# Kernel optimization log

Measured on AMD Instinct MI355X. Metric: run time of the kernel, lower is better.

Reference implementation:

```python
import jax, jax.numpy as jnp
import numpy as np

B, N, C_CLASS, C_CHARGE, S_MAX = 128, 256, 5, 3, 300


def setup_inputs() -> dict:
    key = jax.random.key(0)
    ks = jax.random.split(key, 12)
    return {
        "particle_class": jax.random.randint(ks[0], (B, N), 0, C_CLASS),
        "particle_charge": jax.random.randint(ks[1], (B, N), 0, C_CHARGE),
        "n_particles": jax.random.randint(ks[2], (B,), 0, S_MAX),
        "pflow_class_logits": jax.random.normal(ks[3], (B, N, C_CLASS), jnp.float32),
        "pflow_charge_logits": jax.random.normal(ks[4], (B, N, C_CHARGE), jnp.float32),
        "particle_pos": jax.random.normal(ks[5], (B, N, 3), jnp.float32),
        "pflow_pos": jax.random.normal(ks[6], (B, N, 3), jnp.float32),
        "particle_mom": jax.random.normal(ks[7], (B, N, 3), jnp.float32),
        "pflow_mom": jax.random.normal(ks[8], (B, N, 3), jnp.float32),
        "particle_energy": jax.random.normal(ks[9], (B, N), jnp.float32),
        "pflow_energy": jax.random.normal(ks[10], (B, N), jnp.float32),
        "predicted_setsizes": jax.random.normal(ks[11], (B, N, S_MAX), jnp.float32),
    }


def _pairwise_nll(logits, labels):
    # logits: [B, Nq, C] (pflow/dst side), labels: [B, Np] int (particle/src side)
    # returns CE(dst_logits_j, src_label_i) for every pair -> [B, Np, Nq]
    logp = jax.nn.log_softmax(logits, axis=-1)            # [B, Nq, C]
    idx = labels[:, :, None, None]                        # [B, Np, 1, 1]
    return -jnp.take_along_axis(logp[:, None, :, :], idx, axis=3)[..., 0]


def reference(particle_class, particle_charge, n_particles,
              pflow_class_logits, pflow_charge_logits,
              particle_pos, pflow_pos, particle_mom, pflow_mom,
              particle_energy, pflow_energy, predicted_setsizes):
    # per-edge (full bipartite per event) pair losses -> [B, Np, Nq]
    class_l = _pairwise_nll(pflow_class_logits, particle_class)
    charge_l = _pairwise_nll(pflow_charge_logits, particle_charge)
    pos_l = jnp.linalg.norm(particle_pos[:, :, None, :] - pflow_pos[:, None, :, :], axis=-1)
    mom_l = jnp.linalg.norm(particle_mom[:, :, None, :] - pflow_mom[:, None, :, :], axis=-1)
    en_l = (particle_energy[:, :, None] - pflow_energy[:, None, :]) ** 2
    pair_loss = class_l + charge_l + pos_l + mom_l + en_l  # [B, Np, Nq]

    # segment-min over mailbox: per-pflow min over incoming particle edges,
    # per-particle min over incoming pflow edges
    min_per_pflow = pair_loss.min(axis=1)      # [B, Nq]
    min_per_particle = pair_loss.min(axis=2)   # [B, Np]

    particle_loss = min_per_particle.sum(axis=1).mean()
    pflow_loss = min_per_pflow.sum(axis=1).mean()

    # setsize: mean over pflow nodes per event, CE against true multiplicity
    setsize_logp = jax.nn.log_softmax(predicted_setsizes.mean(axis=1), axis=-1)  # [B, S]
    setsize_loss = -jnp.take_along_axis(setsize_logp, n_particles[:, None], axis=1)[:, 0].mean()

    loss = particle_loss + pflow_loss + setsize_loss
    return loss
```

## Files before the change

kernel.cpp:

```cpp
#include <hip/hip_runtime.h>
#include <math.h>

#define BQ 128
#define NQ 256
#define SMAX 300
#define CCLS 5
#define CCHG 3
#define TSTR 268
#define RSTR 12
#define INFV 3.0e38f

#define NPAIRBLK 512
#define NTHREADS 512

__device__ __forceinline__ float fast_sqrtf(float x) {
    return __builtin_amdgcn_sqrtf(x);
}

#define SMEM_FLOATS 7636

__global__ __launch_bounds__(NTHREADS) void fused_kernel(
    const int* __restrict__ p_class, const int* __restrict__ p_charge,
    const int* __restrict__ n_particles,
    const float* __restrict__ cls_logits, const float* __restrict__ chg_logits,
    const float* __restrict__ p_pos, const float* __restrict__ pf_pos,
    const float* __restrict__ p_mom, const float* __restrict__ pf_mom,
    const float* __restrict__ p_en, const float* __restrict__ pf_en,
    const float* __restrict__ setsizes, float* __restrict__ out)
{
    __shared__ float smem[SMEM_FLOATS];
    const int t = threadIdx.x;
    const int blk = blockIdx.x;

    if (blk < NPAIRBLK) {
        const int b   = blk >> 2;
        const int dir = (blk >> 1) & 1;
        const int rh  = blk & 1;
        const int base = b * NQ;
        float* s_tabT = smem;
        float* s_cols = smem + 4020;
        float* s_rows = smem + 6068;
        float* s_part = smem + 7604;

        if (t < NQ) {
            const int gj = base + t;
            const float* cl = cls_logits + (size_t)gj * CCLS;
            float l0=cl[0], l1=cl[1], l2=cl[2], l3=cl[3], l4=cl[4];
            float mx = fmaxf(fmaxf(fmaxf(l0,l1),fmaxf(l2,l3)),l4);
            float lse = mx + __logf(__expf(l0-mx)+__expf(l1-mx)+__expf(l2-mx)+
                                    __expf(l3-mx)+__expf(l4-mx));
            const float* gl = chg_logits + (size_t)gj * CCHG;
            float g0=gl[0], g1=gl[1], g2=gl[2];
            float gmx = fmaxf(fmaxf(g0,g1),g2);
            float glse = gmx + __logf(__expf(g0-gmx)+__expf(g1-gmx)+__expf(g2-gmx));
            float nc[CCLS] = {lse-l0, lse-l1, lse-l2, lse-l3, lse-l4};
            float ng[CCHG] = {glse-g0, glse-g1, glse-g2};
            #pragma unroll
            for (int c = 0; c < CCLS; ++c)
                #pragma unroll
                for (int g = 0; g < CCHG; ++g)
                    s_tabT[(c*CCHG+g)*TSTR + t] = nc[c] + ng[g];

            const float* cpos = dir ? p_pos : pf_pos;
            const float* cmom = dir ? p_mom : pf_mom;
            const float* cen  = dir ? p_en  : pf_en;
            float* cr = &s_cols[t*8];
            cr[0]=cpos[gj*3+0]; cr[1]=cpos[gj*3+1]; cr[2]=cpos[gj*3+2];
            cr[3]=cmom[gj*3+0]; cr[4]=cmom[gj*3+1]; cr[5]=cmom[gj*3+2];
            cr[6]=cen[gj];
            cr[7]= dir ? __int_as_float(p_class[gj]*CCHG + p_charge[gj]) : 0.0f;
        } else if (t < NQ + 128) {
            const int rr = t - NQ;
            const int gr = base + rh*128 + rr;
            const float* rpos = dir ? pf_pos : p_pos;
            const float* rmom = dir ? pf_mom : p_mom;
            const float* ren  = dir ? pf_en  : p_en;
            float* rw = &s_rows[rr*RSTR];
            rw[0]=rpos[gr*3+0]; rw[1]=rpos[gr*3+1]; rw[2]=rpos[gr*3+2];
            rw[3]=rmom[gr*3+0]; rw[4]=rmom[gr*3+1]; rw[5]=rmom[gr*3+2];
            rw[6]=ren[gr];
            rw[7]= dir ? 0.0f : __int_as_float(p_class[gr]*CCHG + p_charge[gr]);
        }
        __syncthreads();

        const int tx = t & 31;
        const int ty = t >> 5;
        const int c0 = ty * 16;

        float4 ra[4], rb[4];
        int ccr[4];
        #pragma unroll
        for (int r = 0; r < 4; ++r) {
            const int rr = tx + 32*r;
            ra[r] = *(const float4*)&s_rows[rr*RSTR];
            rb[r] = *(const float4*)&s_rows[rr*RSTR + 4];
            ccr[r] = __float_as_int(rb[r].w) * TSTR;
        }
        float rmin[4] = {INFV, INFV, INFV, INFV};

        if (dir == 0) {
            #pragma unroll
            for (int cs = 0; cs < 4; ++cs) {
                float4 tb[4];
                #pragma unroll
                for (int r = 0; r < 4; ++r)
                    tb[r] = *(const float4*)&s_tabT[ccr[r] + c0 + cs*4];
                #pragma unroll
                for (int c = 0; c < 4; ++c) {
                    const int j = c0 + cs*4 + c;
                    const float4 cd0 = *(const float4*)&s_cols[j*8];
                    const float4 cd1 = *(const float4*)&s_cols[j*8+4];
                    #pragma unroll
                    for (int r = 0; r < 4; ++r) {
                        float dx=ra[r].x-cd0.x, dy=ra[r].y-cd0.y, dz=ra[r].z-cd0.z;
                        float ex=ra[r].w-cd0.w, ey=rb[r].x-cd1.x, ez=rb[r].y-cd1.y;
                        float de=rb[r].z-cd1.z;
                        float v = ((const float*)&tb[r])[c]
                                + fast_sqrtf(dx*dx + dy*dy + dz*dz)
                                + fast_sqrtf(ex*ex + ey*ey + ez*ez)
                                + de*de;
                        rmin[r] = fminf(rmin[r], v);
                    }
                }
            }
        } else {
            #pragma unroll
            for (int c16 = 0; c16 < 16; ++c16) {
                const int i = c0 + c16;
                const float4 cd0 = *(const float4*)&s_cols[i*8];
                const float4 cd1 = *(const float4*)&s_cols[i*8+4];
                const float* tabp = &s_tabT[__float_as_int(cd1.w)*TSTR + rh*128 + tx];
                #pragma unroll
                for (int r = 0; r < 4; ++r) {
                    float dx=ra[r].x-cd0.x, dy=ra[r].y-cd0.y, dz=ra[r].z-cd0.z;
                    float ex=ra[r].w-cd0.w, ey=rb[r].x-cd1.x, ez=rb[r].y-cd1.y;
                    float de=rb[r].z-cd1.z;
                    float v = tabp[32*r]
                            + fast_sqrtf(dx*dx + dy*dy + dz*dz)
                            + fast_sqrtf(ex*ex + ey*ey + ez*ez)
                            + de*de;
                    rmin[r] = fminf(rmin[r], v);
                }
            }
        }

        __syncthreads();
        float* s_red = smem;
        #pragma unroll
        for (int r = 0; r < 4; ++r)
            s_red[ty*128 + tx + 32*r] = rmin[r];
        __syncthreads();
        if (t < 128) {
            float m = s_red[t];
            #pragma unroll
            for (int k = 1; k < 16; ++k) m = fminf(m, s_red[k*128 + t]);
            #pragma unroll
            for (int off = 32; off > 0; off >>= 1) m += __shfl_down(m, off);
            if ((t & 63) == 0) s_part[t >> 6] = m;
        }
        __syncthreads();
        if (t == 0) atomicAdd(out, (s_part[0] + s_part[1]) * (1.0f / BQ));

    } else {
        const int b = blk - NPAIRBLK;
        float* s_ss = smem;
        float* s_m  = smem + 608;
        float* s_p5 = smem + 912;
        float* s_one= smem + 920;

        const int slice = t >> 8;
        const int col = t & 255;
        const float* bp = setsizes + (size_t)b * NQ * SMAX + (size_t)(slice*128) * SMAX;
        {
            const float* p = bp + col;
            float acc = 0.f;
            #pragma unroll 8
            for (int i = 0; i < 128; ++i) acc += p[(size_t)i * SMAX];
            s_ss[slice*304 + col] = acc;
        }
        if (col < SMAX - NQ) {
            const float* p = bp + (NQ + col);
            float acc = 0.f;
            #pragma unroll 8
            for (int i = 0; i < 128; ++i) acc += p[(size_t)i * SMAX];
            s_ss[slice*304 + NQ + col] = acc;
        }
        __syncthreads();
        float m = -INFV;
        if (t < SMAX) { m = (s_ss[t] + s_ss[304 + t]) * (1.0f / NQ); s_m[t] = m; }
        const int wave = t >> 6, lane = t & 63;
        float wm = m;
        #pragma unroll
        for (int off = 32; off > 0; off >>= 1) wm = fmaxf(wm, __shfl_down(wm, off));
        if (lane == 0 && wave < 5) s_p5[wave] = wm;
        __syncthreads();
        if (t == 0)
            s_one[0] = fmaxf(fmaxf(fmaxf(s_p5[0], s_p5[1]), fmaxf(s_p5[2], s_p5[3])), s_p5[4]);
        __syncthreads();
        const float mx = s_one[0];
        float e = (t < SMAX) ? __expf(m - mx) : 0.f;
        #pragma unroll
        for (int off = 32; off > 0; off >>= 1) e += __shfl_down(e, off);
        if (lane == 0 && wave < 5) s_p5[wave] = e;
        __syncthreads();
        if (t == 0) {
            float s = s_p5[0] + s_p5[1] + s_p5[2] + s_p5[3] + s_p5[4];
            int nb = n_particles[b];
            float loss = -(s_m[nb] - mx - __logf(s));
            atomicAdd(out, loss * (1.0f / BQ));
        }
    }
}

extern "C" void kernel_launch(void* const* d_in, const int* in_sizes, int n_in,
                              void* d_out, int out_size, void* d_ws, size_t ws_size,
                              hipStream_t stream) {
    (void)in_sizes; (void)n_in; (void)d_ws; (void)ws_size;
    const int*   p_class     = (const int*)d_in[0];
    const int*   p_charge    = (const int*)d_in[1];
    const int*   n_particles = (const int*)d_in[2];
    const float* cls_logits  = (const float*)d_in[3];
    const float* chg_logits  = (const float*)d_in[4];
    const float* p_pos       = (const float*)d_in[5];
    const float* pf_pos      = (const float*)d_in[6];
    const float* p_mom       = (const float*)d_in[7];
    const float* pf_mom      = (const float*)d_in[8];
    const float* p_en        = (const float*)d_in[9];
    const float* pf_en       = (const float*)d_in[10];
    const float* setsizes    = (const float*)d_in[11];
    float* out = (float*)d_out;

    (void)hipMemsetAsync(out, 0, sizeof(float) * (size_t)out_size, stream);

    fused_kernel<<<NPAIRBLK + BQ, NTHREADS, 0, stream>>>(
        p_class, p_charge, n_particles, cls_logits, chg_logits,
        p_pos, pf_pos, p_mom, pf_mom, p_en, pf_en, setsizes, out);
}
```

Measured before the change: 117.5 us.

## Compute row and column mins in one pass per event

Instead of four blocks per event (two directions times two row halves), each recomputing the pair loss, one block per event evaluates every pair once and tracks both per-row and per-column minima. Column minima are reduced with 32-lane shuffles before the final sum. This halves the pairwise sqrt work and cuts the pair-block count from 512 to 128, at the cost of less parallelism on a large GPU and more registers per thread. The setsize loop unroll also goes from 8 to 16.

```diff
diff --git a/kernel.cpp b/kernel.cpp
--- a/kernel.cpp
+++ b/kernel.cpp
@@ -9,15 +9,13 @@
 #define TSTR 268
 #define RSTR 12
 #define INFV 3.0e38f
-
-#define NPAIRBLK 512
 #define NTHREADS 512
 
 __device__ __forceinline__ float fast_sqrtf(float x) {
     return __builtin_amdgcn_sqrtf(x);
 }
 
-#define SMEM_FLOATS 7636
+#define SMEM_FLOATS 9156
 
 __global__ __launch_bounds__(NTHREADS) void fused_kernel(
     const int* __restrict__ p_class, const int* __restrict__ p_charge,
@@ -32,15 +30,13 @@
     const int t = threadIdx.x;
     const int blk = blockIdx.x;
 
-    if (blk < NPAIRBLK) {
-        const int b   = blk >> 2;
-        const int dir = (blk >> 1) & 1;
-        const int rh  = blk & 1;
+    if (blk < BQ) {
+        const int b = blk;
         const int base = b * NQ;
-        float* s_tabT = smem;
+        float* s_tab  = smem;
         float* s_cols = smem + 4020;
         float* s_rows = smem + 6068;
-        float* s_part = smem + 7604;
+        float* s_part = smem + 9140;
 
         if (t < NQ) {
             const int gj = base + t;
@@ -59,27 +55,20 @@
             for (int c = 0; c < CCLS; ++c)
                 #pragma unroll
                 for (int g = 0; g < CCHG; ++g)
-                    s_tabT[(c*CCHG+g)*TSTR + t] = nc[c] + ng[g];
-
-            const float* cpos = dir ? p_pos : pf_pos;
-            const float* cmom = dir ? p_mom : pf_mom;
-            const float* cen  = dir ? p_en  : pf_en;
+                    s_tab[(c*CCHG+g)*TSTR + t] = nc[c] + ng[g];
+
             float* cr = &s_cols[t*8];
-            cr[0]=cpos[gj*3+0]; cr[1]=cpos[gj*3+1]; cr[2]=cpos[gj*3+2];
-            cr[3]=cmom[gj*3+0]; cr[4]=cmom[gj*3+1]; cr[5]=cmom[gj*3+2];
-            cr[6]=cen[gj];
-            cr[7]= dir ? __int_as_float(p_class[gj]*CCHG + p_charge[gj]) : 0.0f;
-        } else if (t < NQ + 128) {
+            cr[0]=pf_pos[gj*3+0]; cr[1]=pf_pos[gj*3+1]; cr[2]=pf_pos[gj*3+2];
+            cr[3]=pf_mom[gj*3+0]; cr[4]=pf_mom[gj*3+1]; cr[5]=pf_mom[gj*3+2];
+            cr[6]=pf_en[gj];      cr[7]=0.0f;
+        } else {
             const int rr = t - NQ;
-            const int gr = base + rh*128 + rr;
-            const float* rpos = dir ? pf_pos : p_pos;
-            const float* rmom = dir ? pf_mom : p_mom;
-            const float* ren  = dir ? pf_en  : p_en;
+            const int gr = base + rr;
             float* rw = &s_rows[rr*RSTR];
-            rw[0]=rpos[gr*3+0]; rw[1]=rpos[gr*3+1]; rw[2]=rpos[gr*3+2];
-            rw[3]=rmom[gr*3+0]; rw[4]=rmom[gr*3+1]; rw[5]=rmom[gr*3+2];
-            rw[6]=ren[gr];
-            rw[7]= dir ? 0.0f : __int_as_float(p_class[gr]*CCHG + p_charge[gr]);
+            rw[0]=p_pos[gr*3+0]; rw[1]=p_pos[gr*3+1]; rw[2]=p_pos[gr*3+2];
+            rw[3]=p_mom[gr*3+0]; rw[4]=p_mom[gr*3+1]; rw[5]=p_mom[gr*3+2];
+            rw[6]=p_en[gr];
+            rw[7]=__int_as_float(p_class[gr]*CCHG + p_charge[gr]);
         }
         __syncthreads();
 
@@ -87,82 +76,80 @@
         const int ty = t >> 5;
         const int c0 = ty * 16;
 
-        float4 ra[4], rb[4];
-        int ccr[4];
-        #pragma unroll
-        for (int r = 0; r < 4; ++r) {
-            const int rr = tx + 32*r;
-            ra[r] = *(const float4*)&s_rows[rr*RSTR];
-            rb[r] = *(const float4*)&s_rows[rr*RSTR + 4];
-            ccr[r] = __float_as_int(rb[r].w) * TSTR;
-        }
-        float rmin[4] = {INFV, INFV, INFV, INFV};
-
-        if (dir == 0) {
-            #pragma unroll
-            for (int cs = 0; cs < 4; ++cs) {
-                float4 tb[4];
-                #pragma unroll
-                for (int r = 0; r < 4; ++r)
-                    tb[r] = *(const float4*)&s_tabT[ccr[r] + c0 + cs*4];
-                #pragma unroll
-                for (int c = 0; c < 4; ++c) {
-                    const int j = c0 + cs*4 + c;
-                    const float4 cd0 = *(const float4*)&s_cols[j*8];
-                    const float4 cd1 = *(const float4*)&s_cols[j*8+4];
-                    #pragma unroll
-                    for (int r = 0; r < 4; ++r) {
-                        float dx=ra[r].x-cd0.x, dy=ra[r].y-cd0.y, dz=ra[r].z-cd0.z;
-                        float ex=ra[r].w-cd0.w, ey=rb[r].x-cd1.x, ez=rb[r].y-cd1.y;
-                        float de=rb[r].z-cd1.z;
-                        float v = ((const float*)&tb[r])[c]
-                                + fast_sqrtf(dx*dx + dy*dy + dz*dz)
-                                + fast_sqrtf(ex*ex + ey*ey + ez*ez)
-                                + de*de;
-                        rmin[r] = fminf(rmin[r], v);
-                    }
-                }
+        float cmin[16];
+        #pragma unroll
+        for (int c = 0; c < 16; ++c) cmin[c] = INFV;
+        float rmins[2][4];
+
+        #pragma unroll
+        for (int p = 0; p < 2; ++p) {
+            float4 ra[4], rb[4];
+            int ccr[4];
+            #pragma unroll
+            for (int r = 0; r < 4; ++r) {
+                const int row = p*128 + tx + 32*r;
+                ra[r] = *(const float4*)&s_rows[row*RSTR];
+                rb[r] = *(const float4*)&s_rows[row*RSTR + 4];
+                ccr[r] = __float_as_int(rb[r].w) * TSTR;
             }
-        } else {
-            #pragma unroll
-            for (int c16 = 0; c16 < 16; ++c16) {
-                const int i = c0 + c16;
-                const float4 cd0 = *(const float4*)&s_cols[i*8];
-                const float4 cd1 = *(const float4*)&s_cols[i*8+4];
-                const float* tabp = &s_tabT[__float_as_int(cd1.w)*TSTR + rh*128 + tx];
+            float rmin[4] = {INFV, INFV, INFV, INFV};
+            #pragma unroll
+            for (int c = 0; c < 16; ++c) {
+                const int j = c0 + c;
+                const float4 cd0 = *(const float4*)&s_cols[j*8];
+                const float4 cd1 = *(const float4*)&s_cols[j*8+4];
+                float cm = cmin[c];
                 #pragma unroll
                 for (int r = 0; r < 4; ++r) {
                     float dx=ra[r].x-cd0.x, dy=ra[r].y-cd0.y, dz=ra[r].z-cd0.z;
                     float ex=ra[r].w-cd0.w, ey=rb[r].x-cd1.x, ez=rb[r].y-cd1.y;
                     float de=rb[r].z-cd1.z;
-                    float v = tabp[32*r]
+                    float v = s_tab[ccr[r] + j]
                             + fast_sqrtf(dx*dx + dy*dy + dz*dz)
                             + fast_sqrtf(ex*ex + ey*ey + ez*ez)
                             + de*de;
                     rmin[r] = fminf(rmin[r], v);
+                    cm = fminf(cm, v);
                 }
+                cmin[c] = cm;
             }
+            #pragma unroll
+            for (int r = 0; r < 4; ++r) rmins[p][r] = rmin[r];
         }
 
         __syncthreads();
         float* s_red = smem;
-        #pragma unroll
-        for (int r = 0; r < 4; ++r)
-            s_red[ty*128 + tx + 32*r] = rmin[r];
-        __syncthreads();
-        if (t < 128) {
+        float* s_cm  = smem + 4224;
+
+        #pragma unroll
+        for (int c = 0; c < 16; ++c) {
+            float v = cmin[c];
+            #pragma unroll
+            for (int off = 16; off > 0; off >>= 1)
+                v = fminf(v, __shfl_down(v, off, 32));
+            if (tx == 0) s_cm[c0 + c] = v;
+        }
+        #pragma unroll
+        for (int r = 0; r < 4; ++r) {
+            s_red[ty*256 + tx + 32*r]        = rmins[0][r];
+            s_red[ty*256 + 128 + tx + 32*r]  = rmins[1][r];
+        }
+        __syncthreads();
+        if (t < NQ) {
             float m = s_red[t];
             #pragma unroll
-            for (int k = 1; k < 16; ++k) m = fminf(m, s_red[k*128 + t]);
-            #pragma unroll
-            for (int off = 32; off > 0; off >>= 1) m += __shfl_down(m, off);
-            if ((t & 63) == 0) s_part[t >> 6] = m;
-        }
-        __syncthreads();
-        if (t == 0) atomicAdd(out, (s_part[0] + s_part[1]) * (1.0f / BQ));
+            for (int k = 1; k < 16; ++k) m = fminf(m, s_red[k*256 + t]);
+            float su = m + s_cm[t];
+            #pragma unroll
+            for (int off = 32; off > 0; off >>= 1) su += __shfl_down(su, off, 64);
+            if ((t & 63) == 0) s_part[t >> 6] = su;
+        }
+        __syncthreads();
+        if (t == 0)
+            atomicAdd(out, (s_part[0]+s_part[1]+s_part[2]+s_part[3]) * (1.0f/BQ));
 
     } else {
-        const int b = blk - NPAIRBLK;
+        const int b = blk - BQ;
         float* s_ss = smem;
         float* s_m  = smem + 608;
         float* s_p5 = smem + 912;
@@ -174,14 +161,14 @@
         {
             const float* p = bp + col;
             float acc = 0.f;
-            #pragma unroll 8
+            #pragma unroll 16
             for (int i = 0; i < 128; ++i) acc += p[(size_t)i * SMAX];
             s_ss[slice*304 + col] = acc;
         }
         if (col < SMAX - NQ) {
             const float* p = bp + (NQ + col);
             float acc = 0.f;
-            #pragma unroll 8
+            #pragma unroll 16
             for (int i = 0; i < 128; ++i) acc += p[(size_t)i * SMAX];
             s_ss[slice*304 + NQ + col] = acc;
         }
@@ -232,7 +219,7 @@
 
     (void)hipMemsetAsync(out, 0, sizeof(float) * (size_t)out_size, stream);
 
-    fused_kernel<<<NPAIRBLK + BQ, NTHREADS, 0, stream>>>(
+    fused_kernel<<<2 * BQ, NTHREADS, 0, stream>>>(
         p_class, p_charge, n_particles, cls_logits, chg_logits,
         p_pos, pf_pos, p_mom, pf_mom, p_en, pf_en, setsizes, out);
 }
```

Measured after the change: 171.4 us. 1.46x slower.
